# Optimization experiments

Measured on AMD Instinct MI355X. Metric: run time of the kernel, lower is better.

Reference implementation:

```python
import jax, jax.numpy as jnp
import numpy as np

N_NODES = 100000
N_EDGES = 3200000
N_FEAT = 128
HIDDEN = 64
N_CLASSES = 3
N_GRAPHS = 512
BN_EPS = 1e-5


def setup_inputs() -> dict:
    key = jax.random.key(0)
    ks = jax.random.split(key, 16)
    x = jax.random.normal(ks[0], (N_NODES, N_FEAT), dtype=jnp.float32)
    edge_index = jax.random.randint(ks[1], (2, N_EDGES), 0, N_NODES, dtype=jnp.int64)
    batch = jnp.sort(jax.random.randint(ks[2], (N_NODES,), 0, N_GRAPHS, dtype=jnp.int64))
    # GCNConv weights (glorot-ish scale), biases
    W1 = jax.random.normal(ks[3], (N_FEAT, HIDDEN), dtype=jnp.float32) / np.sqrt(N_FEAT)
    b1 = jnp.zeros((HIDDEN,), dtype=jnp.float32)
    W2 = jax.random.normal(ks[4], (HIDDEN, HIDDEN), dtype=jnp.float32) / np.sqrt(HIDDEN)
    b2 = jnp.zeros((HIDDEN,), dtype=jnp.float32)
    # BatchNorm params + running stats (eval mode)
    g1 = jnp.ones((HIDDEN,), dtype=jnp.float32)
    bt1 = jnp.zeros((HIDDEN,), dtype=jnp.float32)
    rm1 = jax.random.normal(ks[5], (HIDDEN,), dtype=jnp.float32) * 0.1
    rv1 = jax.random.uniform(ks[6], (HIDDEN,), dtype=jnp.float32) + 0.5
    g2 = jnp.ones((HIDDEN,), dtype=jnp.float32)
    bt2 = jnp.zeros((HIDDEN,), dtype=jnp.float32)
    rm2 = jax.random.normal(ks[7], (HIDDEN,), dtype=jnp.float32) * 0.1
    rv2 = jax.random.uniform(ks[8], (HIDDEN,), dtype=jnp.float32) + 0.5
    # classifier
    Wc = jax.random.normal(ks[9], (HIDDEN, N_CLASSES), dtype=jnp.float32) / np.sqrt(HIDDEN)
    bc = jnp.zeros((N_CLASSES,), dtype=jnp.float32)
    return dict(x=x, W1=W1, b1=b1, g1=g1, bt1=bt1, rm1=rm1, rv1=rv1,
                W2=W2, b2=b2, g2=g2, bt2=bt2, rm2=rm2, rv2=rv2,
                Wc=Wc, bc=bc, edge_index=edge_index, batch=batch)


def _gcn_conv(x, W, b, src, dst):
    # x' = D^{-1/2} (A + I) D^{-1/2} X W + b  (PyG GCNConv with self-loops)
    n = x.shape[0]
    h = x @ W  # [N, H]
    loops = jnp.arange(n, dtype=src.dtype)
    s = jnp.concatenate([src, loops])
    d = jnp.concatenate([dst, loops])
    deg = jax.ops.segment_sum(jnp.ones_like(d, dtype=h.dtype), d, num_segments=n)
    dinv = jnp.where(deg > 0, jax.lax.rsqrt(deg), 0.0)
    norm = dinv[s] * dinv[d]  # [E+N]
    msg = h[s] * norm[:, None]  # gather + scale
    out = jax.ops.segment_sum(msg, d, num_segments=n)  # scatter-add
    return out + b


def _bn_eval(x, gamma, beta, rmean, rvar):
    return (x - rmean) * jax.lax.rsqrt(rvar + BN_EPS) * gamma + beta


def reference(x, W1, b1, g1, bt1, rm1, rv1, W2, b2, g2, bt2, rm2, rv2, Wc, bc, edge_index, batch):
    src, dst = edge_index[0], edge_index[1]
    h = _gcn_conv(x, W1, b1, src, dst)
    h = jax.nn.relu(_bn_eval(h, g1, bt1, rm1, rv1))
    # dropout inactive in eval mode
    h = _gcn_conv(h, W2, b2, src, dst)
    h = jax.nn.relu(_bn_eval(h, g2, bt2, rm2, rv2))
    # global mean pool over graphs
    sums = jax.ops.segment_sum(h, batch, num_segments=N_GRAPHS)
    cnts = jax.ops.segment_sum(jnp.ones((h.shape[0],), dtype=h.dtype), batch, num_segments=N_GRAPHS)
    pooled = sums / jnp.maximum(cnts, 1.0)[:, None]  # [G, H]
    return pooled @ Wc + bc  # [G, C]
```

## Files before the change

kernel.cpp:

```cpp
#include <hip/hip_runtime.h>

#define NN 100000
#define NE 3200000
#define NG 512
#define NCB 391
#define BN_EPS 1e-5f

typedef unsigned short u16;
typedef unsigned int u32;

__device__ __forceinline__ u16 f2bf(float f) {
    u32 u = __float_as_uint(f);
    u += 0x7FFF + ((u >> 16) & 1);
    return (u16)(u >> 16);
}

__global__ __launch_bounds__(256) void k_chist(const int* __restrict__ dst, int* __restrict__ ccount) {
    __shared__ int h[NCB];
    int t = threadIdx.x;
    for (int i = t; i < NCB; i += 256) h[i] = 0;
    __syncthreads();
    int stride = gridDim.x * 256;
    for (int e = blockIdx.x * 256 + t; e < NE; e += stride)
        atomicAdd(&h[dst[e] >> 8], 1);
    __syncthreads();
    for (int i = t; i < NCB; i += 256)
        if (h[i]) atomicAdd(&ccount[i], h[i]);
}

__global__ __launch_bounds__(256) void k_cscan(const int* __restrict__ ccount, int* __restrict__ cbase,
                                               int* __restrict__ fbase, int* __restrict__ gcur) {
    __shared__ int sh[256], sh2[256];
    int t = threadIdx.x;
    int v[2], w[2];
    int s = 0, s2 = 0;
#pragma unroll
    for (int j = 0; j < 2; j++) {
        int idx = t * 2 + j;
        int c = (idx < NCB) ? ccount[idx] : 0;
        v[j] = c;
        w[j] = (idx < NCB) ? ((c + 771) & ~3) : 0;
        s += v[j]; s2 += w[j];
    }
    sh[t] = s; sh2[t] = s2;
    __syncthreads();
    for (int off = 1; off < 256; off <<= 1) {
        int x = (t >= off) ? sh[t - off] : 0;
        int x2 = (t >= off) ? sh2[t - off] : 0;
        __syncthreads();
        sh[t] += x; sh2[t] += x2;
        __syncthreads();
    }
    int run = sh[t] - s, run2 = sh2[t] - s2;
#pragma unroll
    for (int j = 0; j < 2; j++) {
        int idx = t * 2 + j;
        if (idx < NCB) { cbase[idx] = run; gcur[idx] = run; fbase[idx] = run2; }
        run += v[j]; run2 += w[j];
    }
    if (t == 255) cbase[NCB] = run;
}

#define P1_CHUNK 8192
__global__ __launch_bounds__(1024) void k_p1(const int* __restrict__ src, const int* __restrict__ dst,
                                             int* __restrict__ gcur, int* __restrict__ esc) {
    __shared__ int ccur[NCB];
    const int t = threadIdx.x;
    const int e0 = blockIdx.x * P1_CHUNK;
    if (t < NCB) ccur[t] = 0;
    __syncthreads();
    int n = NE - e0; if (n > P1_CHUNK) n = P1_CHUNK;
    for (int idx = t; idx < n; idx += 1024)
        atomicAdd(&ccur[dst[e0 + idx] >> 8], 1);
    __syncthreads();
    if (t < NCB) {
        int c = ccur[t];
        ccur[t] = (c > 0) ? atomicAdd(&gcur[t], c) : 0;
    }
    __syncthreads();
    for (int idx = t; idx < n; idx += 1024) {
        int dd = dst[e0 + idx];
        int s = src[e0 + idx];
        int pos = atomicAdd(&ccur[dd >> 8], 1);
        esc[pos] = s | ((dd & 255) << 17);
    }
}

__global__ __launch_bounds__(256) void k_p2(const int* __restrict__ esc, const int* __restrict__ cbase,
                                            const int* __restrict__ fbase, int* __restrict__ esf,
                                            int* __restrict__ offs, int* __restrict__ cntp,
                                            float* __restrict__ dinv) {
    __shared__ int lcnt[256], sh[256], lcur[256];
    int t = threadIdx.x, b = blockIdx.x;
    int c0 = cbase[b], c1 = cbase[b + 1];
    lcnt[t] = 0;
    __syncthreads();
    for (int i = c0 + t; i < c1; i += 256) atomicAdd(&lcnt[esc[i] >> 17], 1);
    __syncthreads();
    int cnt = lcnt[t];
    int p = (cnt + 3) & ~3;
    sh[t] = p;
    __syncthreads();
    for (int off = 1; off < 256; off <<= 1) {
        int x = (t >= off) ? sh[t - off] : 0;
        __syncthreads();
        sh[t] += x;
        __syncthreads();
    }
    int fb = fbase[b];
    int o = fb + sh[t] - p;
    lcur[t] = o;
    int node = (b << 8) + t;
    if (node < NN) {
        offs[node] = o;
        cntp[node] = p;
        dinv[node] = rsqrtf((float)(cnt + 1));
        for (int q = cnt; q < p; q++) esf[o + q] = NN;
    }
    __syncthreads();
    for (int i = c0 + t; i < c1; i += 256) {
        int rec = esc[i];
        int pos = atomicAdd(&lcur[rec >> 17], 1);
        esf[pos] = rec & 0x1FFFF;
    }
}

template <int K>
__global__ __launch_bounds__(256) void k_gemm(const float* __restrict__ X,
                                              const float* __restrict__ W,
                                              const float* __restrict__ dinv,
                                              u16* __restrict__ hp, int M) {
    __shared__ float ws[K * 64];
    const int t = threadIdx.x;
    const int row0 = blockIdx.x * 256;
    const int rg = t >> 3;
    const int f0 = (t & 7) * 8;

    const float4* Wg = (const float4*)W;
    float4* ws4 = (float4*)ws;
#pragma unroll
    for (int i = 0; i < (K * 16) / 256; i++) ws4[t + i * 256] = Wg[t + i * 256];
    __syncthreads();

    float acc[8][8];
#pragma unroll
    for (int j = 0; j < 8; j++)
#pragma unroll
        for (int c = 0; c < 8; c++) acc[j][c] = 0.0f;

    const float* xr[8];
#pragma unroll
    for (int j = 0; j < 8; j++) {
        int row = row0 + rg + 32 * j;
        xr[j] = X + (size_t)(row < M ? row : 0) * K;
    }

    for (int kk = 0; kk < K; kk += 4) {
        float4 xv[8];
#pragma unroll
        for (int j = 0; j < 8; j++) xv[j] = *(const float4*)(xr[j] + kk);
#pragma unroll
        for (int kki = 0; kki < 4; kki++) {
            float4 w0 = *(const float4*)(&ws[(kk + kki) * 64 + f0]);
            float4 w1 = *(const float4*)(&ws[(kk + kki) * 64 + f0 + 4]);
#pragma unroll
            for (int j = 0; j < 8; j++) {
                float a = (&xv[j].x)[kki];
                acc[j][0] = fmaf(a, w0.x, acc[j][0]);
                acc[j][1] = fmaf(a, w0.y, acc[j][1]);
                acc[j][2] = fmaf(a, w0.z, acc[j][2]);
                acc[j][3] = fmaf(a, w0.w, acc[j][3]);
                acc[j][4] = fmaf(a, w1.x, acc[j][4]);
                acc[j][5] = fmaf(a, w1.y, acc[j][5]);
                acc[j][6] = fmaf(a, w1.z, acc[j][6]);
                acc[j][7] = fmaf(a, w1.w, acc[j][7]);
            }
        }
    }

#pragma unroll
    for (int j = 0; j < 8; j++) {
        int row = row0 + rg + 32 * j;
        if (row < M) {
            float di = dinv[row];
            uint4 pk;
            pk.x = (u32)f2bf(acc[j][0] * di) | ((u32)f2bf(acc[j][1] * di) << 16);
            pk.y = (u32)f2bf(acc[j][2] * di) | ((u32)f2bf(acc[j][3] * di) << 16);
            pk.z = (u32)f2bf(acc[j][4] * di) | ((u32)f2bf(acc[j][5] * di) << 16);
            pk.w = (u32)f2bf(acc[j][6] * di) | ((u32)f2bf(acc[j][7] * di) << 16);
            *(uint4*)(hp + (size_t)row * 64 + f0) = pk;
        }
    }
}

__global__ __launch_bounds__(256) void k_agg(const u32* __restrict__ hp2,
                                             const int* __restrict__ esf,
                                             const int* __restrict__ offs,
                                             const int* __restrict__ cntp,
                                             const float* __restrict__ dinv,
                                             const float* __restrict__ bias,
                                             const float* __restrict__ gam,
                                             const float* __restrict__ bet,
                                             const float* __restrict__ rm,
                                             const float* __restrict__ rv,
                                             float* __restrict__ out) {
    const int lane = threadIdx.x & 63;
    const int half = lane >> 5;
    const int fp = lane & 31;
    const int node = (blockIdx.x * 256 + threadIdx.x) >> 6;
    if (node >= NN) return;
    const int beg = offs[node];
    const int mp = cntp[node];
    float ax = 0.0f, ay = 0.0f;
    for (int c = 0; c < mp; c += 64) {
        int m = mp - c;
        if (m > 64) m = 64;
        int rec = (lane < m) ? esf[beg + c + lane] : NN;
        int j = 0;
        for (; j + 16 <= m; j += 16) {
            u32 v[8];
#pragma unroll
            for (int u = 0; u < 8; u++) {
                int s = __shfl(rec, j + 2 * u + half);
                v[u] = hp2[(size_t)s * 32 + fp];
            }
#pragma unroll
            for (int u = 0; u < 8; u++) {
                ax += __uint_as_float(v[u] << 16);
                ay += __uint_as_float(v[u] & 0xFFFF0000u);
            }
        }
        for (; j < m; j += 4) {
            int s0 = __shfl(rec, j + half);
            int s1 = __shfl(rec, j + 2 + half);
            u32 v0 = hp2[(size_t)s0 * 32 + fp];
            u32 v1 = hp2[(size_t)s1 * 32 + fp];
            ax += __uint_as_float(v0 << 16);
            ay += __uint_as_float(v0 & 0xFFFF0000u);
            ax += __uint_as_float(v1 << 16);
            ay += __uint_as_float(v1 & 0xFFFF0000u);
        }
    }
    ax += __shfl_xor(ax, 32);
    ay += __shfl_xor(ay, 32);
    u32 sv = hp2[(size_t)node * 32 + fp];
    ax += __uint_as_float(sv << 16);
    ay += __uint_as_float(sv & 0xFFFF0000u);

    const float di = dinv[node];
    const int f0 = fp * 2;
    float2 bia = *(const float2*)(bias + f0);
    float2 ga  = *(const float2*)(gam + f0);
    float2 be  = *(const float2*)(bet + f0);
    float2 rme = *(const float2*)(rm + f0);
    float2 rva = *(const float2*)(rv + f0);
    float vx = ax * di + bia.x;
    float vy = ay * di + bia.y;
    float yx = (vx - rme.x) * (ga.x * rsqrtf(rva.x + BN_EPS)) + be.x;
    float yy = (vy - rme.y) * (ga.y * rsqrtf(rva.y + BN_EPS)) + be.y;
    if (half == 0)
        *(float2*)(out + (size_t)node * 64 + f0) = make_float2(fmaxf(yx, 0.0f), fmaxf(yy, 0.0f));
}

__global__ __launch_bounds__(256) void k_poolcls(const float* __restrict__ h,
                                                 const int* __restrict__ batch,
                                                 const float* __restrict__ Wc,
                                                 const float* __restrict__ bc,
                                                 float* __restrict__ out) {
    __shared__ float sh[256];
    const int g = blockIdx.x;
    const int t = threadIdx.x;
    const int lane = t & 63;
    const int wv = t >> 6;
    int lo = 0, hi = NN;
    while (lo < hi) { int mid = (lo + hi) >> 1; if (batch[mid] < g) lo = mid + 1; else hi = mid; }
    const int r0 = lo;
    hi = NN;
    while (lo < hi) { int mid = (lo + hi) >> 1; if (batch[mid] < g + 1) lo = mid + 1; else hi = mid; }
    const int r1 = lo;
    float acc = 0.0f;
    for (int r = r0 + wv; r < r1; r += 4)
        acc += h[(size_t)r * 64 + lane];
    sh[t] = acc;
    __syncthreads();
    if (wv == 0) {
        float p = sh[lane] + sh[64 + lane] + sh[128 + lane] + sh[192 + lane];
        p *= 1.0f / fmaxf((float)(r1 - r0), 1.0f);
        float c0 = p * Wc[lane * 3 + 0];
        float c1 = p * Wc[lane * 3 + 1];
        float c2 = p * Wc[lane * 3 + 2];
        for (int o = 32; o > 0; o >>= 1) {
            c0 += __shfl_xor(c0, o);
            c1 += __shfl_xor(c1, o);
            c2 += __shfl_xor(c2, o);
        }
        if (lane == 0) {
            out[g * 3 + 0] = c0 + bc[0];
            out[g * 3 + 1] = c1 + bc[1];
            out[g * 3 + 2] = c2 + bc[2];
        }
    }
}

extern "C" void kernel_launch(void* const* d_in, const int* in_sizes, int n_in,
                              void* d_out, int out_size, void* d_ws, size_t ws_size,
                              hipStream_t stream) {
    const float* x   = (const float*)d_in[0];
    const float* W1  = (const float*)d_in[1];
    const float* b1  = (const float*)d_in[2];
    const float* g1  = (const float*)d_in[3];
    const float* bt1 = (const float*)d_in[4];
    const float* rm1 = (const float*)d_in[5];
    const float* rv1 = (const float*)d_in[6];
    const float* W2  = (const float*)d_in[7];
    const float* b2  = (const float*)d_in[8];
    const float* g2  = (const float*)d_in[9];
    const float* bt2 = (const float*)d_in[10];
    const float* rm2 = (const float*)d_in[11];
    const float* rv2 = (const float*)d_in[12];
    const float* Wc  = (const float*)d_in[13];
    const float* bc  = (const float*)d_in[14];
    const int* ei    = (const int*)d_in[15];
    const int* batch = (const int*)d_in[16];
    const int* srcp = ei;
    const int* dstp = ei + NE;

    char* ws = (char*)d_ws;
    u16*   hpb    = (u16*)(ws);
    int*   ccount = (int*)(ws + 12800128);
    int*   cbase  = (int*)(ws + 12803264);
    int*   fbase  = (int*)(ws + 12806400);
    int*   gcur   = (int*)(ws + 12809536);
    int*   offs   = (int*)(ws + 12812672);
    int*   cntp   = (int*)(ws + 13212672);
    float* dinv   = (float*)(ws + 13612672);
    int*   esf    = (int*)(ws + 14012672);
    float* bufB   = (float*)(ws + 28052672);
    int*   esc    = (int*)(ws + 28052672);

    hipMemsetAsync(hpb + (size_t)NN * 64, 0, 128 + NCB * 4, stream);

    k_chist<<<512, 256, 0, stream>>>(dstp, ccount);
    k_cscan<<<1, 256, 0, stream>>>(ccount, cbase, fbase, gcur);
    k_p1<<<(NE + P1_CHUNK - 1) / P1_CHUNK, 1024, 0, stream>>>(srcp, dstp, gcur, esc);
    k_p2<<<NCB, 256, 0, stream>>>(esc, cbase, fbase, esf, offs, cntp, dinv);

    k_gemm<128><<<(NN + 255) / 256, 256, 0, stream>>>(x, W1, dinv, hpb, NN);
    k_agg<<<(NN * 64 + 255) / 256, 256, 0, stream>>>((const u32*)hpb, esf, offs, cntp, dinv, b1, g1, bt1, rm1, rv1, bufB);

    k_gemm<64><<<(NN + 255) / 256, 256, 0, stream>>>(bufB, W2, dinv, hpb, NN);
    k_agg<<<(NN * 64 + 255) / 256, 256, 0, stream>>>((const u32*)hpb, esf, offs, cntp, dinv, b2, g2, bt2, rm2, rv2, bufB);

    k_poolcls<<<NG, 256, 0, stream>>>(bufB, batch, Wc, bc, (float*)d_out);
}
```

Baseline: 403.5 us.

## Stage bucketed edges in LDS before global write; shrink GEMM rows per block

The partition kernel now scatters each chunk's edges into a shared-memory buffer sorted by bucket, then writes them to global memory in bucket order so that runs of consecutive addresses replace scattered single stores. A block-level prefix scan computes the local bucket offsets. Separately, each GEMM block now covers 64 rows instead of 256, giving about four times as many blocks for better occupancy and load spread, at the cost of reloading the W tile into shared memory more often. The added shared memory (about 50KB) in the partition kernel may reduce its occupancy.

Result: slower. 537.6 us (+33.2%).

```diff
diff --git a/kernel.cpp b/kernel.cpp
--- a/kernel.cpp
+++ b/kernel.cpp
@@ -65,6 +65,11 @@
 __global__ __launch_bounds__(1024) void k_p1(const int* __restrict__ src, const int* __restrict__ dst,
                                              int* __restrict__ gcur, int* __restrict__ esc) {
     __shared__ int ccur[NCB];
+    __shared__ int lstart[NCB];
+    __shared__ int gbase[NCB];
+    __shared__ int sc[512];
+    __shared__ int lbuf[P1_CHUNK];
+    __shared__ u16 lbkt[P1_CHUNK];
     const int t = threadIdx.x;
     const int e0 = blockIdx.x * P1_CHUNK;
     if (t < NCB) ccur[t] = 0;
@@ -73,16 +78,34 @@
     for (int idx = t; idx < n; idx += 1024)
         atomicAdd(&ccur[dst[e0 + idx] >> 8], 1);
     __syncthreads();
+    int cnt = 0;
+    if (t < 512) { cnt = (t < NCB) ? ccur[t] : 0; sc[t] = cnt; }
+    __syncthreads();
+    for (int off = 1; off < 512; off <<= 1) {
+        int x = (t >= off && t < 512) ? sc[t - off] : 0;
+        __syncthreads();
+        if (t < 512) sc[t] += x;
+        __syncthreads();
+    }
     if (t < NCB) {
-        int c = ccur[t];
-        ccur[t] = (c > 0) ? atomicAdd(&gcur[t], c) : 0;
+        int ls = sc[t] - cnt;
+        lstart[t] = ls;
+        ccur[t] = ls;
+        gbase[t] = (cnt > 0) ? atomicAdd(&gcur[t], cnt) : 0;
     }
     __syncthreads();
     for (int idx = t; idx < n; idx += 1024) {
         int dd = dst[e0 + idx];
         int s = src[e0 + idx];
-        int pos = atomicAdd(&ccur[dd >> 8], 1);
-        esc[pos] = s | ((dd & 255) << 17);
+        int b = dd >> 8;
+        int pos = atomicAdd(&ccur[b], 1);
+        lbuf[pos] = s | ((dd & 255) << 17);
+        lbkt[pos] = (u16)b;
+    }
+    __syncthreads();
+    for (int p = t; p < n; p += 1024) {
+        int b = lbkt[p];
+        esc[gbase[b] + (p - lstart[b])] = lbuf[p];
     }
 }
 
@@ -132,7 +155,7 @@
                                               u16* __restrict__ hp, int M) {
     __shared__ float ws[K * 64];
     const int t = threadIdx.x;
-    const int row0 = blockIdx.x * 256;
+    const int row0 = blockIdx.x * 64;
     const int rg = t >> 3;
     const int f0 = (t & 7) * 8;
 
@@ -142,29 +165,29 @@
     for (int i = 0; i < (K * 16) / 256; i++) ws4[t + i * 256] = Wg[t + i * 256];
     __syncthreads();
 
-    float acc[8][8];
-#pragma unroll
-    for (int j = 0; j < 8; j++)
+    float acc[2][8];
+#pragma unroll
+    for (int j = 0; j < 2; j++)
 #pragma unroll
         for (int c = 0; c < 8; c++) acc[j][c] = 0.0f;
 
-    const float* xr[8];
-#pragma unroll
-    for (int j = 0; j < 8; j++) {
+    const float* xr[2];
+#pragma unroll
+    for (int j = 0; j < 2; j++) {
         int row = row0 + rg + 32 * j;
         xr[j] = X + (size_t)(row < M ? row : 0) * K;
     }
 
     for (int kk = 0; kk < K; kk += 4) {
-        float4 xv[8];
-#pragma unroll
-        for (int j = 0; j < 8; j++) xv[j] = *(const float4*)(xr[j] + kk);
+        float4 xv[2];
+#pragma unroll
+        for (int j = 0; j < 2; j++) xv[j] = *(const float4*)(xr[j] + kk);
 #pragma unroll
         for (int kki = 0; kki < 4; kki++) {
             float4 w0 = *(const float4*)(&ws[(kk + kki) * 64 + f0]);
             float4 w1 = *(const float4*)(&ws[(kk + kki) * 64 + f0 + 4]);
 #pragma unroll
-            for (int j = 0; j < 8; j++) {
+            for (int j = 0; j < 2; j++) {
                 float a = (&xv[j].x)[kki];
                 acc[j][0] = fmaf(a, w0.x, acc[j][0]);
                 acc[j][1] = fmaf(a, w0.y, acc[j][1]);
@@ -179,7 +202,7 @@
     }
 
 #pragma unroll
-    for (int j = 0; j < 8; j++) {
+    for (int j = 0; j < 2; j++) {
         int row = row0 + rg + 32 * j;
         if (row < M) {
             float di = dinv[row];
@@ -345,10 +368,10 @@
     k_p1<<<(NE + P1_CHUNK - 1) / P1_CHUNK, 1024, 0, stream>>>(srcp, dstp, gcur, esc);
     k_p2<<<NCB, 256, 0, stream>>>(esc, cbase, fbase, esf, offs, cntp, dinv);
 
-    k_gemm<128><<<(NN + 255) / 256, 256, 0, stream>>>(x, W1, dinv, hpb, NN);
+    k_gemm<128><<<(NN + 63) / 64, 256, 0, stream>>>(x, W1, dinv, hpb, NN);
     k_agg<<<(NN * 64 + 255) / 256, 256, 0, stream>>>((const u32*)hpb, esf, offs, cntp, dinv, b1, g1, bt1, rm1, rv1, bufB);
 
-    k_gemm<64><<<(NN + 255) / 256, 256, 0, stream>>>(bufB, W2, dinv, hpb, NN);
+    k_gemm<64><<<(NN + 63) / 64, 256, 0, stream>>>(bufB, W2, dinv, hpb, NN);
     k_agg<<<(NN * 64 + 255) / 256, 256, 0, stream>>>((const u32*)hpb, esf, offs, cntp, dinv, b2, g2, bt2, rm2, rv2, bufB);
 
     k_poolcls<<<NG, 256, 0, stream>>>(bufB, batch, Wc, bc, (float*)d_out);
```
